# Optimization experiments

Hardware: AMD Instinct MI355X
Metric: run time of the kernel (lower is better)

Reference implementation:

```python
import jax, jax.numpy as jnp
import numpy as np

NB_ATOMS = 128
NB_CH = 1
ATOM = 12          # atom_size
BATCH = 8
HW = 75            # -> 64x64 patch grid
LAM = 0.1          # soft-threshold level of the L1 proximal
UNROLL = 2         # unroll_steps
FISTA_ITERS = 15   # fixed inner FISTA iterations (replaces res-based stop)


def _prox(u):
    # soft-thresholding (prox of lam*||.||_1)
    return jnp.sign(u) * jnp.maximum(jnp.abs(u) - LAM, 0.0)


def _conv(x, w):
    # valid cross-correlation, NCHW / OIHW (== F.conv2d)
    return jax.lax.conv_general_dilated(x, w, (1, 1), 'VALID',
                                        dimension_numbers=('NCHW', 'OIHW', 'NCHW'))


def _fold(patches, H, W):
    # patches: [B, Ph, Pw, a, a] -> overlap-add to [B, 1, H, W] (== F.fold)
    B, Ph, Pw, a, _ = patches.shape
    out = jnp.zeros((B, H, W), patches.dtype)
    for di in range(a):              # fixed small kernel loop (a*a = 144 slots)
        for dj in range(a):
            out = out.at[:, di:di + Ph, dj:dj + Pw].add(patches[:, :, :, di, dj])
    return out[:, None]


def _fista(c0, X, q, mu):
    # standard FISTA on 0.5*||D^T c - y_patch||^2 + lam*||c||_1 with step mu
    def body(i, st):
        c, z, t = st
        cn = _prox(z - (z @ X - q) * mu)
        tn = (1.0 + jnp.sqrt(1.0 + 4.0 * t * t)) / 2.0
        zn = cn + ((t - 1.0) / tn) * (cn - c)
        return (cn, zn, tn)
    c, _, _ = jax.lax.fori_loop(0, FISTA_ITERS, body, (c0, c0, jnp.float32(1.0)))
    return c


def setup_inputs() -> dict:
    key = jax.random.key(0)
    k1, k2 = jax.random.split(key)
    y = jax.random.normal(k1, (BATCH, NB_CH, HW, HW), dtype=jnp.float32)
    atoms = jax.random.normal(k2, (NB_ATOMS, NB_CH, ATOM, ATOM), dtype=jnp.float32) / 1500.0
    beta = jnp.float32(0.1)
    mu = jnp.float32(1.0)
    return {"y": y, "atoms": atoms, "beta": beta, "mu": mu}


def reference(y, atoms, beta, mu):
    B, C, H, W = y.shape
    N, a = atoms.shape[0], atoms.shape[-1]
    beta = jax.nn.relu(beta)
    mu = jax.nn.relu(mu)
    # normalize atoms: zero-mean, unit L2 rows, then spectral norm / sqrt(mu)
    A = atoms - atoms.mean(axis=(1, 2, 3), keepdims=True)
    Af = A.reshape(N, -1)
    Af = Af / jnp.linalg.norm(Af, axis=1, keepdims=True)
    Af = Af / (jnp.linalg.norm(Af, ord=2) * jnp.sqrt(mu))
    atoms_n = Af.reshape(N, C, a, a)
    X = Af @ Af.T                                   # [N, N] gram
    Ph, Pw = H - a + 1, W - a + 1
    n_patch = B * Ph * Pw
    mean_filter = jnp.ones((1, 1, a, a), y.dtype) / (a * a)
    patch_mean = _conv(y, mean_filter).reshape(n_patch, 1, 1, 1)
    divisors = _fold(jnp.ones((B, Ph, Pw, a, a), y.dtype), H, W)  # overlap counts
    goal = y
    c = jnp.zeros((n_patch, N), y.dtype)
    sg = jax.lax.stop_gradient
    for _ in range(UNROLL):
        q = _conv(goal, atoms_n).transpose(0, 2, 3, 1).reshape(n_patch, N)
        cf = sg(_fista(sg(c), sg(X), sg(q), sg(mu)))   # torch.no_grad inner solve
        cf = _prox(cf - (cf @ X - q) * mu)             # one differentiable step
        pred = jnp.einsum('pn,ncij->pcij', cf, atoms_n) + patch_mean  # [P,1,a,a]
        pred = _fold(pred.reshape(B, Ph, Pw, a, a), H, W)
        goal = (y + beta * pred) / (1.0 + beta * divisors)
        c = cf
    return goal
```

## Files before the change

### kernel.cpp

```cpp
#include <hip/hip_runtime.h>
#include <stdint.h>

#define AA 144
#define LAM 0.1f

#define OFS_SC    0
#define OFS_AF1   64
#define OFS_G     36928
#define OFS_S0    53312
#define OFS_S1    69696
#define OFS_X     86080
#define OFS_PM    139328
#define OFS_GOAL  172096
#define OFS_CF    4411456
#define OFS_PRED  8605760
#define OFS_ATB   OFS_S0
#define OFS_ANTB  OFS_S1


typedef __attribute__((ext_vector_type(8))) short short8_t;
typedef __attribute__((ext_vector_type(4))) float f32x4;
typedef __attribute__((ext_vector_type(2))) float f32x2;

__device__ __forceinline__ unsigned short f2bf(float f) {
    union { float f; uint32_t u; } x; x.f = f;
    uint32_t u = x.u;
    return (unsigned short)((u + 0x7FFFu + ((u >> 16) & 1u)) >> 16);
}
__device__ __forceinline__ unsigned short f2bh(float f) {
    union { float f; uint32_t u; } x; x.f = f;
    return (unsigned short)((x.u + 0x8000u) >> 16);
}
__device__ __forceinline__ float bf2f(unsigned short u) {
    union { float f; uint32_t i; } x; x.i = ((uint32_t)u) << 16; return x.f;
}
__device__ __forceinline__ uint32_t pack_bf(float a, float b) {
    union { float f; uint32_t u; } xa, xb; xa.f = a; xb.f = b;
    return __builtin_amdgcn_perm(xb.u + 0x8000u, xa.u + 0x8000u, 0x07060302u);
}

#define PSTR 136
__global__ __launch_bounds__(1024) void k_setup(const float* atoms, const float* mu_p,
                                                float* ws, const float* y) {
    __shared__ unsigned short ABf[128 * 168];
    __shared__ unsigned short Pb[2][128 * PSTR];
    __shared__ float tr_arr[10];
    __shared__ float v[128];
    __shared__ float red[256];
    int t = threadIdx.x;
    if (blockIdx.x != 0) {
        int e = (blockIdx.x - 1) * 1024 + t;
        if (e < 45000) ws[OFS_GOAL + e] = y[e];
        if (e < 32768) {
            int b = e >> 12, pi = (e >> 6) & 63, pj = e & 63;
            const float* yb = y + b * 5625;
            float s = 0.f;
            for (int di = 0; di < 12; ++di) {
                const float* row = yb + (pi + di) * 75 + pj;
                #pragma unroll
                for (int dj = 0; dj < 12; ++dj) s += row[dj];
            }
            ws[OFS_PM + e] = s * (1.0f / 144.0f);
        }
        return;
    }
    int lane = t & 63, w = t >> 6;
    int col = lane & 15, quad = lane >> 4;
    if (t < 10) tr_arr[t] = (t == 0) ? 128.0f : 0.f;

    {
        int a = t >> 3, sub = t & 7;
        const float* ap = atoms + a * AA + sub * 18;
        float s = 0.f;
        #pragma unroll
        for (int k = 0; k < 18; ++k) s += ap[k];
        s += __shfl_xor(s, 1, 8); s += __shfl_xor(s, 2, 8); s += __shfl_xor(s, 4, 8);
        float mean = s * (1.0f / 144.0f);
        float ss = 0.f;
        #pragma unroll
        for (int k = 0; k < 18; ++k) { float d = ap[k] - mean; ss = fmaf(d, d, ss); }
        ss += __shfl_xor(ss, 1, 8); ss += __shfl_xor(ss, 2, 8); ss += __shfl_xor(ss, 4, 8);
        float rn = 1.0f / sqrtf(ss);
        #pragma unroll
        for (int k = 0; k < 18; ++k) {
            float av = (ap[k] - mean) * rn;
            ws[OFS_AF1 + a * AA + sub * 18 + k] = av;
            ABf[a * 168 + sub * 18 + k] = f2bf(av);
        }
        if (sub == 0) {
            #pragma unroll
            for (int k = AA; k < 160; ++k) ABf[a * 168 + k] = 0;
        }
    }
    __syncthreads();

    {
        uint32_t* D32 = (uint32_t*)Pb[0];
        float* G = ws + OFS_G;
        int mt = w & 7, gh = w >> 3;
        short8_t af[5];
        #pragma unroll
        for (int s = 0; s < 5; ++s)
            af[s] = *(const short8_t*)&ABf[(mt * 16 + col) * 168 + s * 32 + quad * 8];
        #pragma unroll
        for (int gi = 0; gi < 2; ++gi) {
            int g = gh * 2 + gi;
            short8_t b0[5], b1[5];
            #pragma unroll
            for (int s = 0; s < 5; ++s) {
                b0[s] = *(const short8_t*)&ABf[((2 * g) * 16 + col) * 168 + s * 32 + quad * 8];
                b1[s] = *(const short8_t*)&ABf[((2 * g + 1) * 16 + col) * 168 + s * 32 + quad * 8];
            }
            f32x4 a0 = (f32x4){0.f, 0.f, 0.f, 0.f};
            f32x4 a1 = (f32x4){0.f, 0.f, 0.f, 0.f};
            #pragma unroll
            for (int s = 0; s < 5; ++s) {
                a0 = __builtin_amdgcn_mfma_f32_16x16x32_bf16(af[s], b0[s], a0, 0, 0, 0);
                a1 = __builtin_amdgcn_mfma_f32_16x16x32_bf16(af[s], b1[s], a1, 0, 0, 0);
            }
            #pragma unroll
            for (int r = 0; r < 4; ++r) {
                int m = mt * 16 + quad * 4 + r;
                G[m * 128 + g * 32 + col] = a0[r];
                G[m * 128 + g * 32 + 16 + col] = a1[r];
                D32[m * 68 + g * 16 + col] = pack_bf(a0[r], a1[r]);
            }
        }
    }
    __syncthreads();

    int cur = 0;
    #pragma unroll 1
    for (int j = 0; j < 8; ++j) {
        float trn = tr_arr[j];
        float inv2 = 1.0f / (trn * trn);
        const unsigned short* S = Pb[cur];
        uint32_t* D32 = (uint32_t*)Pb[cur ^ 1];
        int mt = w & 7, nh = w >> 3;
        short8_t af[4];
        #pragma unroll
        for (int s = 0; s < 4; ++s)
            af[s] = *(const short8_t*)&S[(mt * 16 + col) * PSTR + s * 32 + quad * 8];
        #pragma unroll
        for (int pr = 0; pr < 2; ++pr) {
            int ntE = 4 * nh + 2 * pr, ntO = ntE + 1;
            short8_t bE[4], bO[4];
            #pragma unroll
            for (int s = 0; s < 4; ++s) {
                bE[s] = *(const short8_t*)&S[(ntE * 16 + col) * PSTR + s * 32 + quad * 8];
                bO[s] = *(const short8_t*)&S[(ntO * 16 + col) * PSTR + s * 32 + quad * 8];
            }
            f32x4 aE = (f32x4){0.f, 0.f, 0.f, 0.f};
            f32x4 aO = (f32x4){0.f, 0.f, 0.f, 0.f};
            #pragma unroll
            for (int s = 0; s < 4; ++s) {
                aE = __builtin_amdgcn_mfma_f32_16x16x32_bf16(af[s], bE[s], aE, 0, 0, 0);
                aO = __builtin_amdgcn_mfma_f32_16x16x32_bf16(af[s], bO[s], aO, 0, 0, 0);
            }
            int nE = ntE * 16 + col, nO = ntO * 16 + col;
            #pragma unroll
            for (int r = 0; r < 4; ++r) {
                float x0 = aE[r] * inv2, x1 = aO[r] * inv2;
                int row = mt * 16 + quad * 4 + r;
                D32[row * 68 + (ntE >> 1) * 16 + col] = pack_bf(x0, x1);
                if (row == nE) atomicAdd(&tr_arr[j + 1], x0);
                if (row == nO) atomicAdd(&tr_arr[j + 1], x1);
            }
        }
        __syncthreads();
        cur ^= 1;
    }

    {
        int a = t >> 3, sub = t & 7;
        const unsigned short* S = Pb[cur];
        float s = 0.f;
        #pragma unroll
        for (int k = 0; k < 16; ++k) s += bf2f(S[a * PSTR + sub * 16 + k]);
        s += __shfl_xor(s, 1, 8); s += __shfl_xor(s, 2, 8); s += __shfl_xor(s, 4, 8);
        if (sub == 0) v[a] = s;
    }
    __syncthreads();
    {
        int a = t >> 3, sub = t & 7;
        const float* G = ws + OFS_G;
        float wv = 0.f;
        #pragma unroll
        for (int k = 0; k < 16; ++k)
            wv = fmaf(G[a * 128 + sub * 16 + k], v[sub * 16 + k], wv);
        wv += __shfl_xor(wv, 1, 8); wv += __shfl_xor(wv, 2, 8); wv += __shfl_xor(wv, 4, 8);
        if (sub == 0) { red[a] = v[a] * wv; red[128 + a] = v[a] * v[a]; }
    }
    __syncthreads();
    for (int off = 64; off > 0; off >>= 1) {
        if (t < off) { red[t] += red[t + off]; red[128 + t] += red[128 + t + off]; }
        __syncthreads();
    }
    if (t == 0) {
        float lam = red[0] / red[128];
        float mu = fmaxf(mu_p[0], 0.0f);
        ws[OFS_SC + 16] = 1.0f / (lam * mu);
        ws[OFS_SC + 17] = 1.0f / (sqrtf(lam) * sqrtf(mu));
    }
}

__global__ __launch_bounds__(256) void k_finalize(float* ws) {
    int idx = blockIdx.x * 256 + threadIdx.x;
    float scX = ws[OFS_SC + 16], scA = ws[OFS_SC + 17];
    if (idx < 16384) {
        int n = idx >> 7, ks = idx & 127;
        int g = ks >> 5, rem = ks & 31, u = rem >> 1, v = rem & 1;
        int k = g * 32 + v * 16 + u;
        ((unsigned short*)(ws + OFS_X))[idx] = f2bf(ws[OFS_G + n * 128 + k] * scX);
    } else if (idx < 36864) {
        int e = idx - 16384;
        int n = e / 160, k = e - n * 160;
        float v = (k < 144) ? ws[OFS_AF1 + n * 144 + k] * scA : 0.f;
        ((unsigned short*)(ws + OFS_ATB))[e] = f2bf(v);
    } else {
        int e = idx - 36864;
        int jp = e >> 7, ks = e & 127;
        int g = ks >> 5, rem = ks & 31, u = rem >> 1, v = rem & 1;
        int n = g * 32 + v * 16 + u;
        ((unsigned short*)(ws + OFS_ANTB))[e] = f2bf(ws[OFS_AF1 + n * 144 + jp] * scA);
    }
}

__global__ __launch_bounds__(256) void k_fista(const unsigned short* XPB, const float* goal,
                                               const unsigned short* ATB,
                                               const unsigned short* ANTBP,
                                               const float* pm, uint32_t* cfgb,
                                               unsigned short* predh,
                                               const float* mu_p, int first, int write_cf) {
    __shared__ unsigned short Atile[32 * 168];
    __shared__ unsigned short Zbuf[2][32 * 136];
    int t = threadIdx.x;
    int lane = t & 63, w = t >> 6;
    int col = lane & 15, quad = lane >> 4;
    int nb = w * 32;
    int blk = blockIdx.x;
    int b = blk >> 7, pi = (blk >> 1) & 63, h = blk & 1;
    int p0 = blk * 32;
    float mu = fmaxf(mu_p[0], 0.0f);
    const f32x2 mu2 = (f32x2){mu, mu};
    const f32x2 lam2 = (f32x2){LAM, LAM};
    const f32x2 nlam2 = (f32x2){-LAM, -LAM};

    {
        const float* gb = goal + b * 5625 + pi * 75 + h * 32;
        uint32_t* A32 = (uint32_t*)Atile;
        #pragma unroll
        for (int i = 0; i < 10; ++i) {
            int pe = t + i * 256;
            int m = pe / 80, q32 = pe - m * 80;
            int kk = q32 * 2;
            float v0 = 0.f, v1 = 0.f;
            if (kk < 144) {
                int di = kk / 12, dj = kk - di * 12;
                v0 = gb[di * 75 + m + dj];
                int k1 = kk + 1, di1 = k1 / 12, dj1 = k1 - di1 * 12;
                v1 = gb[di1 * 75 + m + dj1];
            }
            A32[m * 84 + q32] = pack_bf(v0, v1);
        }
    }
    __syncthreads();

    f32x2 qv2[2][4];
    {
        short8_t bfq[2][5];
        #pragma unroll
        for (int nt = 0; nt < 2; ++nt)
            #pragma unroll
            for (int s = 0; s < 5; ++s)
                bfq[nt][s] = *(const short8_t*)&ATB[(nb + nt * 16 + col) * 160 + s * 32 + quad * 8];
        #pragma unroll
        for (int mt = 0; mt < 2; ++mt) {
            short8_t af[5];
            #pragma unroll
            for (int s = 0; s < 5; ++s)
                af[s] = *(const short8_t*)&Atile[(mt * 16 + col) * 168 + s * 32 + quad * 8];
            f32x4 acc0 = (f32x4){0.f, 0.f, 0.f, 0.f};
            f32x4 acc1 = (f32x4){0.f, 0.f, 0.f, 0.f};
            #pragma unroll
            for (int s = 0; s < 5; ++s) {
                acc0 = __builtin_amdgcn_mfma_f32_16x16x32_bf16(af[s], bfq[0][s], acc0, 0, 0, 0);
                acc1 = __builtin_amdgcn_mfma_f32_16x16x32_bf16(af[s], bfq[1][s], acc1, 0, 0, 0);
            }
            #pragma unroll
            for (int r = 0; r < 4; ++r) qv2[mt][r] = (f32x2){acc0[r], acc1[r]};
        }
    }

    short8_t xf[2][4];
    #pragma unroll
    for (int nt = 0; nt < 2; ++nt)
        #pragma unroll
        for (int s = 0; s < 4; ++s)
            xf[nt][s] = *(const short8_t*)&XPB[(nb + nt * 16 + col) * 128 + s * 32 + quad * 8];

    uint32_t* Z32w = (uint32_t*)Zbuf[0];
    f32x2 cv2[2][4], zo2[2][4];
    #pragma unroll
    for (int mt = 0; mt < 2; ++mt)
        #pragma unroll
        for (int r = 0; r < 4; ++r) {
            int row = mt * 16 + quad * 4 + r;
            uint32_t pk = 0u;
            float c0 = 0.f, c1 = 0.f;
            if (!first) {
                pk = cfgb[(p0 + row) * 64 + 16 * w + col];
                c0 = bf2f((unsigned short)(pk & 0xFFFFu));
                c1 = bf2f((unsigned short)(pk >> 16));
            }
            cv2[mt][r] = (f32x2){c0, c1};
            zo2[mt][r] = (f32x2){c0, c1};
            Z32w[row * 68 + 16 * w + col] = pk;
        }
    __syncthreads();

    f32x4 acc[2][2];
    auto matmul = [&](const unsigned short* Zr) {
        short8_t af[2][4];
        #pragma unroll
        for (int mt = 0; mt < 2; ++mt)
            #pragma unroll
            for (int s = 0; s < 4; ++s)
                af[mt][s] = *(const short8_t*)&Zr[(mt * 16 + col) * 136 + s * 32 + quad * 8];
        #pragma unroll
        for (int mt = 0; mt < 2; ++mt)
            #pragma unroll
            for (int nt = 0; nt < 2; ++nt)
                acc[mt][nt] = (f32x4){0.f, 0.f, 0.f, 0.f};
        #pragma unroll
        for (int s = 0; s < 4; ++s)
            #pragma unroll
            for (int mt = 0; mt < 2; ++mt)
                #pragma unroll
                for (int nt = 0; nt < 2; ++nt)
                    acc[mt][nt] = __builtin_amdgcn_mfma_f32_16x16x32_bf16(
                        af[mt][s], xf[nt][s], acc[mt][nt], 0, 0, 0);
    };

    float tm = 1.0f;
    int cur = 0;
    #pragma unroll 1
    for (int it = 0; it < 14; ++it) {
        matmul(Zbuf[cur]);
        float tnn = 0.5f * (1.0f + sqrtf(1.0f + 4.0f * tm * tm));
        float fm = (tm - 1.0f) / tnn;
        tm = tnn;
        f32x2 fm2 = (f32x2){fm, fm};
        uint32_t* Zw = (uint32_t*)Zbuf[cur ^ 1];
        #pragma unroll
        for (int mt = 0; mt < 2; ++mt)
            #pragma unroll
            for (int r = 0; r < 4; ++r) {
                f32x2 a2 = (f32x2){acc[mt][0][r], acc[mt][1][r]};
                f32x2 u2 = mu2 * (qv2[mt][r] - a2) + zo2[mt][r];
                f32x2 cl2 = __builtin_elementwise_min(
                                __builtin_elementwise_max(u2, nlam2), lam2);
                f32x2 cn2 = u2 - cl2;
                f32x2 zn2 = fm2 * (cn2 - cv2[mt][r]) + cn2;
                cv2[mt][r] = cn2;
                zo2[mt][r] = zn2;
                Zw[(mt * 16 + quad * 4 + r) * 68 + 16 * w + col] = pack_bf(zn2[0], zn2[1]);
            }
        __syncthreads();
        cur ^= 1;
    }
    {
        matmul(Zbuf[cur]);
        uint32_t* Zw = (uint32_t*)Zbuf[cur ^ 1];
        #pragma unroll
        for (int mt = 0; mt < 2; ++mt)
            #pragma unroll
            for (int r = 0; r < 4; ++r) {
                f32x2 a2 = (f32x2){acc[mt][0][r], acc[mt][1][r]};
                f32x2 u2 = mu2 * (qv2[mt][r] - a2) + zo2[mt][r];
                f32x2 cl2 = __builtin_elementwise_min(
                                __builtin_elementwise_max(u2, nlam2), lam2);
                f32x2 cn2 = u2 - cl2;
                cv2[mt][r] = cn2;
                Zw[(mt * 16 + quad * 4 + r) * 68 + 16 * w + col] = pack_bf(cn2[0], cn2[1]);
            }
        __syncthreads();
        cur ^= 1;
    }
    {
        matmul(Zbuf[cur]);
        uint32_t* Zw = (uint32_t*)Zbuf[cur ^ 1];
        #pragma unroll
        for (int mt = 0; mt < 2; ++mt)
            #pragma unroll
            for (int r = 0; r < 4; ++r) {
                int row = mt * 16 + quad * 4 + r;
                f32x2 a2 = (f32x2){acc[mt][0][r], acc[mt][1][r]};
                f32x2 u2 = mu2 * (qv2[mt][r] - a2) + cv2[mt][r];
                f32x2 cl2 = __builtin_elementwise_min(
                                __builtin_elementwise_max(u2, nlam2), lam2);
                f32x2 cf2 = u2 - cl2;
                uint32_t pk = pack_bf(cf2[0], cf2[1]);
                if (write_cf) cfgb[(p0 + row) * 64 + 16 * w + col] = pk;
                Zw[row * 68 + 16 * w + col] = pk;
            }
        __syncthreads();
        cur ^= 1;
    }

    {
        int jt0 = (w == 0) ? 0 : (2 * w + 1);
        int jtn = (w == 0) ? 3 : 2;
        const unsigned short* Zr = Zbuf[cur];
        short8_t af[2][4];
        #pragma unroll
        for (int mt = 0; mt < 2; ++mt)
            #pragma unroll
            for (int s = 0; s < 4; ++s)
                af[mt][s] = *(const short8_t*)&Zr[(mt * 16 + col) * 136 + s * 32 + quad * 8];
        f32x4 accp[2][3];
        #pragma unroll
        for (int mt = 0; mt < 2; ++mt)
            #pragma unroll
            for (int ji = 0; ji < 3; ++ji)
                accp[mt][ji] = (f32x4){0.f, 0.f, 0.f, 0.f};
        #pragma unroll
        for (int ji = 0; ji < 3; ++ji) {
            if (ji < jtn) {
                int jt = jt0 + ji;
                short8_t bf4[4];
                #pragma unroll
                for (int s = 0; s < 4; ++s)
                    bf4[s] = *(const short8_t*)&ANTBP[(jt * 16 + col) * 128 + s * 32 + quad * 8];
                #pragma unroll
                for (int mt = 0; mt < 2; ++mt)
                    #pragma unroll
                    for (int s = 0; s < 4; ++s)
                        accp[mt][ji] = __builtin_amdgcn_mfma_f32_16x16x32_bf16(
                            af[mt][s], bf4[s], accp[mt][ji], 0, 0, 0);
            }
        }
        #pragma unroll
        for (int mt = 0; mt < 2; ++mt)
            #pragma unroll
            for (int r = 0; r < 4; ++r) {
                int p = p0 + mt * 16 + quad * 4 + r;
                float pmv = pm[p];
                #pragma unroll
                for (int ji = 0; ji < 3; ++ji)
                    if (ji < jtn)
                        predh[p * 144 + (jt0 + ji) * 16 + col] = f2bh(accp[mt][ji][r] + pmv);
            }
    }
}

__global__ __launch_bounds__(256) void k_fold(const float* y, const float* beta_p,
                                              const unsigned short* predh, float* goal,
                                              float* out, int write_out) {
    __shared__ float P[12 * 832];
    int i = blockIdx.x, b = blockIdx.y;
    int t = threadIdx.x;
    for (int di = 0; di < 12; ++di) {
        int pi = i - di;
        if ((unsigned)pi >= 64u) continue;
        int base = (b << 12) + (pi << 6);
        #pragma unroll
        for (int it = 0; it < 3; ++it) {
            int e = t + it * 256;
            int pj = e / 12, dj = e - pj * 12;
            P[di * 832 + pj * 13 + dj] = bf2f(predh[(base + pj) * AA + di * 12 + dj]);
        }
    }
    __syncthreads();
    if (t >= 75) return;
    int j = t;
    float S = 0.f;
    for (int di = 0; di < 12; ++di) {
        if ((unsigned)(i - di) >= 64u) continue;
        const float* Pd = &P[di * 832];
        #pragma unroll
        for (int dj = 0; dj < 12; ++dj) {
            int pj = j - dj;
            if ((unsigned)pj >= 64u) continue;
            S += Pd[pj * 13 + dj];
        }
    }
    int ci = min(i, 11) - max(i - 63, 0) + 1;
    int cj = min(j, 11) - max(j - 63, 0) + 1;
    float beta = fmaxf(beta_p[0], 0.0f);
    int idx = i * 75 + j;
    float yv = y[b * 5625 + idx];
    float g = (yv + beta * S) / (1.0f + beta * (float)(ci * cj));
    if (write_out) out[b * 5625 + idx] = g;
    else           goal[b * 5625 + idx] = g;
}

extern "C" void kernel_launch(void* const* d_in, const int* in_sizes, int n_in,
                              void* d_out, int out_size, void* d_ws, size_t ws_size,
                              hipStream_t stream) {
    const float* y     = (const float*)d_in[0];
    const float* atoms = (const float*)d_in[1];
    const float* beta  = (const float*)d_in[2];
    const float* mu    = (const float*)d_in[3];
    float* out = (float*)d_out;
    float* ws = (float*)d_ws;

    k_setup<<<46, 1024, 0, stream>>>(atoms, mu, ws, y);
    k_finalize<<<216, 256, 0, stream>>>(ws);

    for (int u = 0; u < 2; ++u) {
        k_fista<<<1024, 256, 0, stream>>>((const unsigned short*)(ws + OFS_X),
                                          ws + OFS_GOAL,
                                          (const unsigned short*)(ws + OFS_ATB),
                                          (const unsigned short*)(ws + OFS_ANTB),
                                          ws + OFS_PM, (uint32_t*)(ws + OFS_CF),
                                          (unsigned short*)(ws + OFS_PRED),
                                          mu, u == 0 ? 1 : 0, u == 0 ? 1 : 0);
        k_fold<<<dim3(75, 8), 256, 0, stream>>>(y, beta,
                                                (const unsigned short*)(ws + OFS_PRED),
                                                ws + OFS_GOAL, out, u == 1 ? 1 : 0);
    }
}
```

Baseline: 212.7 us.

## Halve FISTA block patch tile to 16 rows and double grid size

After: 215.3 us. About the same (+1.2%).

```diff
diff --git a/kernel.cpp b/kernel.cpp
--- a/kernel.cpp
+++ b/kernel.cpp
@@ -232,25 +232,27 @@
                                                const float* pm, uint32_t* cfgb,
                                                unsigned short* predh,
                                                const float* mu_p, int first, int write_cf) {
-    __shared__ unsigned short Atile[32 * 168];
-    __shared__ unsigned short Zbuf[2][32 * 136];
+    __shared__ union __align__(16) {
+        unsigned short Atile[16 * 168];
+        unsigned short Zbuf[2][16 * 136];
+    } sm;
     int t = threadIdx.x;
     int lane = t & 63, w = t >> 6;
     int col = lane & 15, quad = lane >> 4;
     int nb = w * 32;
     int blk = blockIdx.x;
-    int b = blk >> 7, pi = (blk >> 1) & 63, h = blk & 1;
-    int p0 = blk * 32;
+    int b = blk >> 8, pi = (blk >> 2) & 63, h = blk & 3;
+    int p0 = blk * 16;
     float mu = fmaxf(mu_p[0], 0.0f);
     const f32x2 mu2 = (f32x2){mu, mu};
     const f32x2 lam2 = (f32x2){LAM, LAM};
     const f32x2 nlam2 = (f32x2){-LAM, -LAM};
 
     {
-        const float* gb = goal + b * 5625 + pi * 75 + h * 32;
-        uint32_t* A32 = (uint32_t*)Atile;
-        #pragma unroll
-        for (int i = 0; i < 10; ++i) {
+        const float* gb = goal + b * 5625 + pi * 75 + h * 16;
+        uint32_t* A32 = (uint32_t*)sm.Atile;
+        #pragma unroll
+        for (int i = 0; i < 5; ++i) {
             int pe = t + i * 256;
             int m = pe / 80, q32 = pe - m * 80;
             int kk = q32 * 2;
@@ -266,7 +268,7 @@
     }
     __syncthreads();
 
-    f32x2 qv2[2][4];
+    f32x2 qv2[4];
     {
         short8_t bfq[2][5];
         #pragma unroll
@@ -274,23 +276,21 @@
             #pragma unroll
             for (int s = 0; s < 5; ++s)
                 bfq[nt][s] = *(const short8_t*)&ATB[(nb + nt * 16 + col) * 160 + s * 32 + quad * 8];
-        #pragma unroll
-        for (int mt = 0; mt < 2; ++mt) {
-            short8_t af[5];
-            #pragma unroll
-            for (int s = 0; s < 5; ++s)
-                af[s] = *(const short8_t*)&Atile[(mt * 16 + col) * 168 + s * 32 + quad * 8];
-            f32x4 acc0 = (f32x4){0.f, 0.f, 0.f, 0.f};
-            f32x4 acc1 = (f32x4){0.f, 0.f, 0.f, 0.f};
-            #pragma unroll
-            for (int s = 0; s < 5; ++s) {
-                acc0 = __builtin_amdgcn_mfma_f32_16x16x32_bf16(af[s], bfq[0][s], acc0, 0, 0, 0);
-                acc1 = __builtin_amdgcn_mfma_f32_16x16x32_bf16(af[s], bfq[1][s], acc1, 0, 0, 0);
-            }
-            #pragma unroll
-            for (int r = 0; r < 4; ++r) qv2[mt][r] = (f32x2){acc0[r], acc1[r]};
-        }
-    }
+        short8_t af[5];
+        #pragma unroll
+        for (int s = 0; s < 5; ++s)
+            af[s] = *(const short8_t*)&sm.Atile[col * 168 + s * 32 + quad * 8];
+        f32x4 acc0 = (f32x4){0.f, 0.f, 0.f, 0.f};
+        f32x4 acc1 = (f32x4){0.f, 0.f, 0.f, 0.f};
+        #pragma unroll
+        for (int s = 0; s < 5; ++s) {
+            acc0 = __builtin_amdgcn_mfma_f32_16x16x32_bf16(af[s], bfq[0][s], acc0, 0, 0, 0);
+            acc1 = __builtin_amdgcn_mfma_f32_16x16x32_bf16(af[s], bfq[1][s], acc1, 0, 0, 0);
+        }
+        #pragma unroll
+        for (int r = 0; r < 4; ++r) qv2[r] = (f32x2){acc0[r], acc1[r]};
+    }
+    __syncthreads();
 
     short8_t xf[2][4];
     #pragma unroll
@@ -299,111 +299,95 @@
         for (int s = 0; s < 4; ++s)
             xf[nt][s] = *(const short8_t*)&XPB[(nb + nt * 16 + col) * 128 + s * 32 + quad * 8];
 
-    uint32_t* Z32w = (uint32_t*)Zbuf[0];
-    f32x2 cv2[2][4], zo2[2][4];
+    uint32_t* Z32w = (uint32_t*)sm.Zbuf[0];
+    f32x2 cv2[4], zo2[4];
     #pragma unroll
-    for (int mt = 0; mt < 2; ++mt)
-        #pragma unroll
-        for (int r = 0; r < 4; ++r) {
-            int row = mt * 16 + quad * 4 + r;
-            uint32_t pk = 0u;
-            float c0 = 0.f, c1 = 0.f;
-            if (!first) {
-                pk = cfgb[(p0 + row) * 64 + 16 * w + col];
-                c0 = bf2f((unsigned short)(pk & 0xFFFFu));
-                c1 = bf2f((unsigned short)(pk >> 16));
-            }
-            cv2[mt][r] = (f32x2){c0, c1};
-            zo2[mt][r] = (f32x2){c0, c1};
-            Z32w[row * 68 + 16 * w + col] = pk;
-        }
-    __syncthreads();
-
-    f32x4 acc[2][2];
+    for (int r = 0; r < 4; ++r) {
+        int row = quad * 4 + r;
+        uint32_t pk = 0u;
+        float c0 = 0.f, c1 = 0.f;
+        if (!first) {
+            pk = cfgb[(p0 + row) * 64 + 16 * w + col];
+            c0 = bf2f((unsigned short)(pk & 0xFFFFu));
+            c1 = bf2f((unsigned short)(pk >> 16));
+        }
+        cv2[r] = (f32x2){c0, c1};
+        zo2[r] = (f32x2){c0, c1};
+        Z32w[row * 68 + 16 * w + col] = pk;
+    }
+    __syncthreads();
+
+    f32x4 acc[2];
     auto matmul = [&](const unsigned short* Zr) {
-        short8_t af[2][4];
-        #pragma unroll
-        for (int mt = 0; mt < 2; ++mt)
-            #pragma unroll
-            for (int s = 0; s < 4; ++s)
-                af[mt][s] = *(const short8_t*)&Zr[(mt * 16 + col) * 136 + s * 32 + quad * 8];
-        #pragma unroll
-        for (int mt = 0; mt < 2; ++mt)
-            #pragma unroll
-            for (int nt = 0; nt < 2; ++nt)
-                acc[mt][nt] = (f32x4){0.f, 0.f, 0.f, 0.f};
+        short8_t af[4];
         #pragma unroll
         for (int s = 0; s < 4; ++s)
-            #pragma unroll
-            for (int mt = 0; mt < 2; ++mt)
-                #pragma unroll
-                for (int nt = 0; nt < 2; ++nt)
-                    acc[mt][nt] = __builtin_amdgcn_mfma_f32_16x16x32_bf16(
-                        af[mt][s], xf[nt][s], acc[mt][nt], 0, 0, 0);
+            af[s] = *(const short8_t*)&Zr[col * 136 + s * 32 + quad * 8];
+        acc[0] = (f32x4){0.f, 0.f, 0.f, 0.f};
+        acc[1] = (f32x4){0.f, 0.f, 0.f, 0.f};
+        #pragma unroll
+        for (int s = 0; s < 4; ++s) {
+            acc[0] = __builtin_amdgcn_mfma_f32_16x16x32_bf16(af[s], xf[0][s], acc[0], 0, 0, 0);
+            acc[1] = __builtin_amdgcn_mfma_f32_16x16x32_bf16(af[s], xf[1][s], acc[1], 0, 0, 0);
+        }
     };
 
     float tm = 1.0f;
     int cur = 0;
     #pragma unroll 1
     for (int it = 0; it < 14; ++it) {
-        matmul(Zbuf[cur]);
+        matmul(sm.Zbuf[cur]);
         float tnn = 0.5f * (1.0f + sqrtf(1.0f + 4.0f * tm * tm));
         float fm = (tm - 1.0f) / tnn;
         tm = tnn;
         f32x2 fm2 = (f32x2){fm, fm};
-        uint32_t* Zw = (uint32_t*)Zbuf[cur ^ 1];
-        #pragma unroll
-        for (int mt = 0; mt < 2; ++mt)
-            #pragma unroll
-            for (int r = 0; r < 4; ++r) {
-                f32x2 a2 = (f32x2){acc[mt][0][r], acc[mt][1][r]};
-                f32x2 u2 = mu2 * (qv2[mt][r] - a2) + zo2[mt][r];
-                f32x2 cl2 = __builtin_elementwise_min(
-                                __builtin_elementwise_max(u2, nlam2), lam2);
-                f32x2 cn2 = u2 - cl2;
-                f32x2 zn2 = fm2 * (cn2 - cv2[mt][r]) + cn2;
-                cv2[mt][r] = cn2;
-                zo2[mt][r] = zn2;
-                Zw[(mt * 16 + quad * 4 + r) * 68 + 16 * w + col] = pack_bf(zn2[0], zn2[1]);
-            }
+        uint32_t* Zw = (uint32_t*)sm.Zbuf[cur ^ 1];
+        #pragma unroll
+        for (int r = 0; r < 4; ++r) {
+            f32x2 a2 = (f32x2){acc[0][r], acc[1][r]};
+            f32x2 u2 = mu2 * (qv2[r] - a2) + zo2[r];
+            f32x2 cl2 = __builtin_elementwise_min(
+                            __builtin_elementwise_max(u2, nlam2), lam2);
+            f32x2 cn2 = u2 - cl2;
+            f32x2 zn2 = fm2 * (cn2 - cv2[r]) + cn2;
+            cv2[r] = cn2;
+            zo2[r] = zn2;
+            Zw[(quad * 4 + r) * 68 + 16 * w + col] = pack_bf(zn2[0], zn2[1]);
+        }
         __syncthreads();
         cur ^= 1;
     }
     {
-        matmul(Zbuf[cur]);
-        uint32_t* Zw = (uint32_t*)Zbuf[cur ^ 1];
-        #pragma unroll
-        for (int mt = 0; mt < 2; ++mt)
-            #pragma unroll
-            for (int r = 0; r < 4; ++r) {
-                f32x2 a2 = (f32x2){acc[mt][0][r], acc[mt][1][r]};
-                f32x2 u2 = mu2 * (qv2[mt][r] - a2) + zo2[mt][r];
-                f32x2 cl2 = __builtin_elementwise_min(
-                                __builtin_elementwise_max(u2, nlam2), lam2);
-                f32x2 cn2 = u2 - cl2;
-                cv2[mt][r] = cn2;
-                Zw[(mt * 16 + quad * 4 + r) * 68 + 16 * w + col] = pack_bf(cn2[0], cn2[1]);
-            }
+        matmul(sm.Zbuf[cur]);
+        uint32_t* Zw = (uint32_t*)sm.Zbuf[cur ^ 1];
+        #pragma unroll
+        for (int r = 0; r < 4; ++r) {
+            f32x2 a2 = (f32x2){acc[0][r], acc[1][r]};
+            f32x2 u2 = mu2 * (qv2[r] - a2) + zo2[r];
+            f32x2 cl2 = __builtin_elementwise_min(
+                            __builtin_elementwise_max(u2, nlam2), lam2);
+            f32x2 cn2 = u2 - cl2;
+            cv2[r] = cn2;
+            Zw[(quad * 4 + r) * 68 + 16 * w + col] = pack_bf(cn2[0], cn2[1]);
+        }
         __syncthreads();
         cur ^= 1;
     }
     {
-        matmul(Zbuf[cur]);
-        uint32_t* Zw = (uint32_t*)Zbuf[cur ^ 1];
-        #pragma unroll
-        for (int mt = 0; mt < 2; ++mt)
-            #pragma unroll
-            for (int r = 0; r < 4; ++r) {
-                int row = mt * 16 + quad * 4 + r;
-                f32x2 a2 = (f32x2){acc[mt][0][r], acc[mt][1][r]};
-                f32x2 u2 = mu2 * (qv2[mt][r] - a2) + cv2[mt][r];
-                f32x2 cl2 = __builtin_elementwise_min(
-                                __builtin_elementwise_max(u2, nlam2), lam2);
-                f32x2 cf2 = u2 - cl2;
-                uint32_t pk = pack_bf(cf2[0], cf2[1]);
-                if (write_cf) cfgb[(p0 + row) * 64 + 16 * w + col] = pk;
-                Zw[row * 68 + 16 * w + col] = pk;
-            }
+        matmul(sm.Zbuf[cur]);
+        uint32_t* Zw = (uint32_t*)sm.Zbuf[cur ^ 1];
+        #pragma unroll
+        for (int r = 0; r < 4; ++r) {
+            int row = quad * 4 + r;
+            f32x2 a2 = (f32x2){acc[0][r], acc[1][r]};
+            f32x2 u2 = mu2 * (qv2[r] - a2) + cv2[r];
+            f32x2 cl2 = __builtin_elementwise_min(
+                            __builtin_elementwise_max(u2, nlam2), lam2);
+            f32x2 cf2 = u2 - cl2;
+            uint32_t pk = pack_bf(cf2[0], cf2[1]);
+            if (write_cf) cfgb[(p0 + row) * 64 + 16 * w + col] = pk;
+            Zw[row * 68 + 16 * w + col] = pk;
+        }
         __syncthreads();
         cur ^= 1;
     }
@@ -411,46 +395,34 @@
     {
         int jt0 = (w == 0) ? 0 : (2 * w + 1);
         int jtn = (w == 0) ? 3 : 2;
-        const unsigned short* Zr = Zbuf[cur];
-        short8_t af[2][4];
-        #pragma unroll
-        for (int mt = 0; mt < 2; ++mt)
-            #pragma unroll
-            for (int s = 0; s < 4; ++s)
-                af[mt][s] = *(const short8_t*)&Zr[(mt * 16 + col) * 136 + s * 32 + quad * 8];
-        f32x4 accp[2][3];
-        #pragma unroll
-        for (int mt = 0; mt < 2; ++mt)
-            #pragma unroll
-            for (int ji = 0; ji < 3; ++ji)
-                accp[mt][ji] = (f32x4){0.f, 0.f, 0.f, 0.f};
+        const unsigned short* Zr = sm.Zbuf[cur];
+        short8_t af[4];
+        #pragma unroll
+        for (int s = 0; s < 4; ++s)
+            af[s] = *(const short8_t*)&Zr[col * 136 + s * 32 + quad * 8];
+        f32x4 accp[3];
+        #pragma unroll
+        for (int ji = 0; ji < 3; ++ji) accp[ji] = (f32x4){0.f, 0.f, 0.f, 0.f};
         #pragma unroll
         for (int ji = 0; ji < 3; ++ji) {
             if (ji < jtn) {
                 int jt = jt0 + ji;
-                short8_t bf4[4];
                 #pragma unroll
-                for (int s = 0; s < 4; ++s)
-                    bf4[s] = *(const short8_t*)&ANTBP[(jt * 16 + col) * 128 + s * 32 + quad * 8];
-                #pragma unroll
-                for (int mt = 0; mt < 2; ++mt)
-                    #pragma unroll
-                    for (int s = 0; s < 4; ++s)
-                        accp[mt][ji] = __builtin_amdgcn_mfma_f32_16x16x32_bf16(
-                            af[mt][s], bf4[s], accp[mt][ji], 0, 0, 0);
-            }
-        }
-        #pragma unroll
-        for (int mt = 0; mt < 2; ++mt)
-            #pragma unroll
-            for (int r = 0; r < 4; ++r) {
-                int p = p0 + mt * 16 + quad * 4 + r;
-                float pmv = pm[p];
-                #pragma unroll
-                for (int ji = 0; ji < 3; ++ji)
-                    if (ji < jtn)
-                        predh[p * 144 + (jt0 + ji) * 16 + col] = f2bh(accp[mt][ji][r] + pmv);
-            }
+                for (int s = 0; s < 4; ++s) {
+                    short8_t bf4 = *(const short8_t*)&ANTBP[(jt * 16 + col) * 128 + s * 32 + quad * 8];
+                    accp[ji] = __builtin_amdgcn_mfma_f32_16x16x32_bf16(af[s], bf4, accp[ji], 0, 0, 0);
+                }
+            }
+        }
+        #pragma unroll
+        for (int r = 0; r < 4; ++r) {
+            int p = p0 + quad * 4 + r;
+            float pmv = pm[p];
+            #pragma unroll
+            for (int ji = 0; ji < 3; ++ji)
+                if (ji < jtn)
+                    predh[p * 144 + (jt0 + ji) * 16 + col] = f2bh(accp[ji][r] + pmv);
+        }
     }
 }
 
@@ -509,7 +481,7 @@
     k_finalize<<<216, 256, 0, stream>>>(ws);
 
     for (int u = 0; u < 2; ++u) {
-        k_fista<<<1024, 256, 0, stream>>>((const unsigned short*)(ws + OFS_X),
+        k_fista<<<2048, 256, 0, stream>>>((const unsigned short*)(ws + OFS_X),
                                           ws + OFS_GOAL,
                                           (const unsigned short*)(ws + OFS_ATB),
                                           (const unsigned short*)(ws + OFS_ANTB),
```
